# Optimization experiments

Measured on AMD Instinct MI355X. Metric: run time of the kernel, lower is better.

## Reference

```python
import jax, jax.numpy as jnp
import numpy as np

D_MODEL = 1024
NUM_HEADS = 16
ROPE_THETA = 10000.0


def setup_inputs() -> dict:
    key = jax.random.key(0)
    ks = jax.random.split(key, 5)
    B, S, D = 4, 2048, D_MODEL
    std = (2.0 / (D * D)) ** 0.5
    return {
        "x": jax.random.normal(ks[0], (B, S, D), dtype=jnp.float32),
        "Wq": jax.random.normal(ks[1], (D, D), dtype=jnp.float32) * std,
        "Wk": jax.random.normal(ks[2], (D, D), dtype=jnp.float32) * std,
        "Wv": jax.random.normal(ks[3], (D, D), dtype=jnp.float32) * std,
        "Wo": jax.random.normal(ks[4], (D, D), dtype=jnp.float32) * std,
    }


def _apply_rope(t, sin, cos):
    # t: [B, H, S, d_k]; sin/cos: [S, d_k//2] (broadcast over B, H)
    e = t[..., 0::2]
    o = t[..., 1::2]
    rot = jnp.stack((e * cos - o * sin, e * sin + o * cos), axis=-1)
    return rot.reshape(t.shape)  # interleave back to d_k


def reference(x, Wq, Wk, Wv, Wo):
    B, S, D = x.shape
    H = NUM_HEADS
    dk = D // H

    def proj(W):
        y = jnp.einsum('bsd,ed->bse', x, W)  # Linear: weight is [out, in]
        return y.reshape(B, S, H, dk).transpose(0, 2, 1, 3)  # [B,H,S,dk]

    q, k, v = proj(Wq), proj(Wk), proj(Wv)

    # RoPE cache (token_positions = arange(S))
    half = dk // 2
    inv_freq = 1.0 / (ROPE_THETA ** (jnp.arange(half, dtype=jnp.float32) * 2.0 / dk))
    angles = jnp.arange(S, dtype=jnp.float32)[:, None] * inv_freq[None, :]  # [S, half]
    sin, cos = jnp.sin(angles), jnp.cos(angles)
    q = _apply_rope(q, sin, cos)
    k = _apply_rope(k, sin, cos)

    # scaled dot-product attention with causal mask
    scores = jnp.einsum('bhqd,bhkd->bhqk', q, k) / jnp.sqrt(jnp.float32(dk))
    causal = jnp.tril(jnp.ones((S, S), dtype=bool))
    scores = jnp.where(causal, scores, jnp.finfo(scores.dtype).min)
    p = jax.nn.softmax(scores, axis=-1)
    out = jnp.einsum('bhqk,bhkd->bhqd', p, v)  # [B,H,S,dk]

    out = out.transpose(0, 2, 1, 3).reshape(B, S, D)
    return jnp.einsum('bsd,ed->bse', out, Wo)
```

## Files before the change

### kernel.cpp

```cpp
#include <hip/hip_runtime.h>

typedef unsigned short u16;
typedef unsigned int   u32;

typedef short    short8 __attribute__((ext_vector_type(8)));
typedef __bf16   bf16x8 __attribute__((ext_vector_type(8)));
typedef _Float16 half8  __attribute__((ext_vector_type(8)));
typedef float    f32x4  __attribute__((ext_vector_type(4)));

#define S_LEN   2048
#define DM      1024
#define NHEAD   16
#define DK      64
#define KDIM    1024

__device__ __forceinline__ u16 f2bf(float f) {
    u32 u = __builtin_bit_cast(u32, f);
    u += 0x7FFFu + ((u >> 16) & 1u);
    return (u16)(u >> 16);
}
__device__ __forceinline__ f32x4 mfma_bf16(short8 a, short8 b, f32x4 c) {
    return __builtin_amdgcn_mfma_f32_16x16x32_bf16(
        __builtin_bit_cast(bf16x8, a), __builtin_bit_cast(bf16x8, b), c, 0, 0, 0);
}
__device__ __forceinline__ f32x4 mfma_f16(half8 a, half8 b, f32x4 c) {
    return __builtin_amdgcn_mfma_f32_16x16x32_f16(a, b, c, 0, 0, 0);
}
__device__ __forceinline__ u32 pk_f16(float a, float b) {
    return __builtin_bit_cast(u32, __builtin_amdgcn_cvt_pkrtz(a, b));
}
__device__ __forceinline__ void gl_lds16(const void* g, void* l) {
    __builtin_amdgcn_global_load_lds(
        (const __attribute__((address_space(1))) u32*)g,
        (__attribute__((address_space(3))) u32*)l, 16, 0, 0);
}
__device__ __forceinline__ void bar_raw() { asm volatile("s_barrier" ::: "memory"); }
__device__ __forceinline__ void wait_vm2() { asm volatile("s_waitcnt vmcnt(2)" ::: "memory"); }
__device__ __forceinline__ void wait_vm0() { asm volatile("s_waitcnt vmcnt(0)" ::: "memory"); }

__device__ __forceinline__ int perm_inv(int rc) {
    const int nt = rc >> 4, mid = (rc >> 2) & 3, r = rc & 3;
    return 32 * (nt >> 1) + 8 * mid + 4 * (nt & 1) + r;
}

__global__ void cvt_all(const float4* __restrict__ x,  const float4* __restrict__ Wq,
                        const float4* __restrict__ Wk, const float4* __restrict__ Wv,
                        const float4* __restrict__ Wo,
                        uint2* __restrict__ oX, uint2* __restrict__ oWcat,
                        uint2* __restrict__ oWo,
                        float* __restrict__ sT, float* __restrict__ cT) {
    const int i = blockIdx.x * 256 + threadIdx.x;
    if (i < 3145728) {
        const float4* in;
        uint2* out;
        if (i < 2097152) {
            in = x + i;  out = oX + i;
        } else {
            const int j = i - 2097152;
            const int w = j >> 18, k = j & 262143;
            in  = (w == 0 ? Wq : w == 1 ? Wk : w == 2 ? Wv : Wo) + k;
            out = (w < 3) ? (oWcat + w * 262144 + k) : (oWo + k);
        }
        float4 f = *in;
        uint2 o;
        o.x = (u32)f2bf(f.x) | ((u32)f2bf(f.y) << 16);
        o.y = (u32)f2bf(f.z) | ((u32)f2bf(f.w) << 16);
        *out = o;
    } else {
        const int idx = i - 3145728;
        const float fi = expf(-(float)(idx >> 11) * 0.287823136624255f);
        const float ang = (float)(idx & 2047) * fi;
        sT[idx] = sinf(ang);
        cT[idx] = cosf(ang);
    }
}

template <int MODE>
__global__ __launch_bounds__(256)
void gemm_nt(const u16* __restrict__ A, const u16* __restrict__ Bw,
             u16* __restrict__ oQ, u16* __restrict__ oK, u16* __restrict__ oVt,
             float* __restrict__ oF,
             const float* __restrict__ ropeS, const float* __restrict__ ropeC) {
    __shared__ u16 As[2][128 * 32];
    __shared__ u16 Bs[2][128 * 32];
    const int tid  = threadIdx.x;
    const int wave = tid >> 6, lane = tid & 63;
    const int quad = lane >> 4, l15 = lane & 15;
    const int wr = wave >> 1, wc = wave & 1;
    const int NX  = (MODE == 0) ? 24 : 8;
    const int lin = (int)blockIdx.x + NX * (int)blockIdx.y;
    const int xcd = lin & 7, idx = lin >> 3;
    const int mbase = (xcd * 8 + idx / NX) * 128;
    const int nbase = (idx % NX) * 128;

    f32x4 acc[4][4];
#pragma unroll
    for (int i = 0; i < 4; i++)
#pragma unroll
        for (int j = 0; j < 4; j++) acc[i][j] = (f32x4)0.0f;

    const int srow0 = wave * 32 + (lane >> 2);
    const int srow1 = srow0 + 16;
    const int scolb = ((lane & 3) ^ ((lane >> 3) & 3)) * 16;
    const int ldsOff = wave * 2048 + lane * 16;
    const u16* gA0 = A  + (size_t)(mbase + srow0) * KDIM;
    const u16* gA1 = A  + (size_t)(mbase + srow1) * KDIM;
    const u16* gB0 = Bw + (size_t)(nbase + srow0) * KDIM;
    const u16* gB1 = Bw + (size_t)(nbase + srow1) * KDIM;
    const int koffq = (quad ^ ((l15 >> 1) & 3)) * 8;

    const int KT = KDIM / 64;
    for (int kt = 0; kt < KT; kt++) {
        const int kk = kt * 64;
        __syncthreads();
#pragma unroll
        for (int s = 0; s < 2; s++) {
            const int ko = kk + s * 32;
            gl_lds16((const char*)(gA0 + ko) + scolb, (char*)As[s] + ldsOff);
            gl_lds16((const char*)(gA1 + ko) + scolb, (char*)As[s] + ldsOff + 1024);
            gl_lds16((const char*)(gB0 + ko) + scolb, (char*)Bs[s] + ldsOff);
            gl_lds16((const char*)(gB1 + ko) + scolb, (char*)Bs[s] + ldsOff + 1024);
        }
        __syncthreads();

        short8 af[4][2], bf[4][2];
#pragma unroll
        for (int s = 0; s < 2; s++) {
#pragma unroll
            for (int mt = 0; mt < 4; mt++)
                af[mt][s] = *(const short8*)&As[s][(wr * 64 + mt * 16 + l15) * 32 + koffq];
#pragma unroll
            for (int nt = 0; nt < 4; nt++)
                bf[nt][s] = *(const short8*)&Bs[s][(wc * 64 + nt * 16 + l15) * 32 + koffq];
        }
#pragma unroll
        for (int s = 0; s < 2; s++)
#pragma unroll
            for (int mt = 0; mt < 4; mt++)
#pragma unroll
                for (int nt = 0; nt < 4; nt++)
                    acc[mt][nt] = mfma_bf16(af[mt][s], bf[nt][s], acc[mt][nt]);
    }

    const int proj_blk = (MODE == 0) ? (nbase >> 10) : 2;

    const float* sB[4];
    const float* cB[4];
    if (MODE == 0 && proj_blk < 2) {
#pragma unroll
        for (int nt = 0; nt < 4; nt++) {
            const int fi = nt * 8 + (l15 >> 1);
            sB[nt] = ropeS + fi * 2048;
            cB[nt] = ropeC + fi * 2048;
        }
    }
    const int par = l15 & 1;

#pragma unroll
    for (int mt = 0; mt < 4; mt++) {
#pragma unroll
        for (int nt = 0; nt < 4; nt++) {
            const int n  = nbase + wc * 64 + nt * 16 + l15;
            const int mb = mbase + wr * 64 + mt * 16 + quad * 4;
            f32x4 v = acc[mt][nt];
            if (MODE == 0) {
                const int e = n & 1023;
                const int h = e >> 6, d = e & 63;
                if (proj_blk == 2) {
                    const int b_ = mb >> 11, s = mb & 2047;
                    const int bh = b_ * NHEAD + h;
                    uint2 pk;
                    pk.x = pk_f16(v[0], v[1]);
                    pk.y = pk_f16(v[2], v[3]);
                    *(uint2*)&oVt[((size_t)bh * DK + d) * S_LEN + s] = pk;
                } else {
                    u16* dst = (proj_blk == 0) ? oQ : oK;
                    float vp[4];
#pragma unroll
                    for (int r = 0; r < 4; r++) vp[r] = __shfl_xor(v[r], 1);
                    const int b_ = mb >> 11, s0 = mb & 2047;
                    const int bh = b_ * NHEAD + h;
                    const f32x4 sn = *(const f32x4*)(sB[nt] + s0);
                    const f32x4 cs = *(const f32x4*)(cB[nt] + s0);
#pragma unroll
                    for (int r = 0; r < 4; r++) {
                        const float res = par ? (vp[r] * sn[r] + v[r] * cs[r])
                                              : (v[r] * cs[r] - vp[r] * sn[r]);
                        dst[((size_t)bh * S_LEN + (s0 + r)) * DK + d] = f2bf(res);
                    }
                }
            } else {
#pragma unroll
                for (int r = 0; r < 4; r++)
                    oF[(size_t)(mb + r) * DM + n] = v[r];
            }
        }
    }
}

__global__ __launch_bounds__(512)
void flash_attn(const u16* __restrict__ Q, const u16* __restrict__ K,
                const u16* __restrict__ Vt, u16* __restrict__ Oc) {
    __shared__ u16 Ks[2][64 * 64];
    __shared__ u16 Vs[2][64 * 64];
    const int lin = (int)blockIdx.x + 64 * (int)blockIdx.y;
    const int xcd = lin & 7, idx = lin >> 3;
    const int bh  = xcd * 8 + (idx & 7);
    const int qt  = 15 - (idx >> 3);
    const int tid  = threadIdx.x;
    const int wave = tid >> 6, lane = tid & 63;
    const int hh   = wave >> 2, w4 = wave & 3;
    const int quad = lane >> 4, l15 = lane & 15;
    const int x7 = l15 & 7;
    const size_t headQK = (size_t)bh * S_LEN * DK;
    const size_t headVt = (size_t)bh * DK * S_LEN;
    const int b = bh >> 4, h = bh & 15;
    const float SCL = 0.18033688011112042f;
    const float THRESH = 44.3614195558365f;

    half8 ones;
#pragma unroll
    for (int j = 0; j < 8; j++) ones[j] = (_Float16)1.0f;

    const int rwl  = lane >> 3;
    const int scol = (lane & 7) ^ rwl;
    const int rc   = wave * 8 + rwl;
    const u16* gK = K  + headQK + (size_t)perm_inv(rc) * DK + scol * 8;
    const u16* gV = Vt + headVt + (size_t)rc * S_LEN + scol * 8;
    const int ldsOff = wave * 1024 + lane * 16;
    const int koff0 = (quad ^ x7) * 8;
    const int koff1 = ((4 + quad) ^ x7) * 8;

    short8 qf0, qf1;
    {
        const int qrow = qt * 128 + hh * 64 + w4 * 16 + l15;
        qf0 = *(const short8*)&Q[headQK + (size_t)qrow * DK + quad * 8];
        qf1 = *(const short8*)&Q[headQK + (size_t)qrow * DK + 32 + quad * 8];
    }

    float m_st = -__builtin_inff();
    f32x4 lacc = (f32x4)0.0f;
    f32x4 oacc[4];
#pragma unroll
    for (int n = 0; n < 4; n++) oacc[n] = (f32x4)0.0f;

    const int NT = 2 * qt + 2;
    const int skip_kt = (hh == 0) ? (2 * qt + 1) : -1;
    const int diag_kt = 2 * qt + hh;
    gl_lds16(gK, (char*)Ks[0] + ldsOff);
    gl_lds16(gV, (char*)Vs[0] + ldsOff);

    for (int kt = 0; kt < NT; kt++) {
        const int cur = kt & 1, nxt = cur ^ 1;
        bar_raw();
        {
            const int ktn = (kt + 1 < NT) ? kt + 1 : kt;
            gl_lds16(gK + (size_t)ktn * 64 * DK, (char*)Ks[nxt] + ldsOff);
            gl_lds16(gV + ktn * 64,              (char*)Vs[nxt] + ldsOff);
        }
        wait_vm2();
        bar_raw();

        if (kt == skip_kt) continue;

        f32x4 sc[4];
        __builtin_amdgcn_s_setprio(1);
#pragma unroll
        for (int nt = 0; nt < 4; nt++) {
            const int rb = (nt * 16 + l15) * 64;
            short8 kf0 = *(const short8*)&Ks[cur][rb + koff0];
            short8 kf1 = *(const short8*)&Ks[cur][rb + koff1];
            f32x4 z = (f32x4)0.0f;
            z = mfma_bf16(kf0, qf0, z);
            z = mfma_bf16(kf1, qf1, z);
            sc[nt] = z;
        }
        __builtin_amdgcn_s_setprio(0);

        if (kt == diag_kt) {
            const int qloc = w4 * 16 + l15;
#pragma unroll
            for (int nt = 0; nt < 4; nt++) {
                const int kb = 32 * (nt >> 1) + 8 * quad + 4 * (nt & 1);
#pragma unroll
                for (int r = 0; r < 4; r++)
                    if (kb + r > qloc) sc[nt][r] = -__builtin_inff();
            }
        }
        float mx0 = fmaxf(fmaxf(sc[0][0], sc[0][1]), fmaxf(sc[0][2], sc[0][3]));
        float mx1 = fmaxf(fmaxf(sc[1][0], sc[1][1]), fmaxf(sc[1][2], sc[1][3]));
        float mx2 = fmaxf(fmaxf(sc[2][0], sc[2][1]), fmaxf(sc[2][2], sc[2][3]));
        float mx3 = fmaxf(fmaxf(sc[3][0], sc[3][1]), fmaxf(sc[3][2], sc[3][3]));
        float mx = fmaxf(fmaxf(mx0, mx1), fmaxf(mx2, mx3));
        mx = fmaxf(mx, __shfl_xor(mx, 16));
        mx = fmaxf(mx, __shfl_xor(mx, 32));
        if (!__all(mx - m_st <= THRESH)) {
            const float mn = fmaxf(m_st, mx);
            const float alpha = __builtin_amdgcn_exp2f((m_st - mn) * SCL);
            m_st = mn;
            float alr[4];
#pragma unroll
            for (int r = 0; r < 4; r++) alr[r] = __shfl(alpha, quad * 20 + r);
#pragma unroll
            for (int n = 0; n < 4; n++)
#pragma unroll
                for (int r = 0; r < 4; r++) oacc[n][r] *= alr[r];
#pragma unroll
            for (int r = 0; r < 4; r++) lacc[r] *= alr[r];
        }
        const float msc = m_st * SCL;
#pragma unroll
        for (int nt = 0; nt < 4; nt++)
#pragma unroll
            for (int r = 0; r < 4; r++)
                sc[nt][r] = __builtin_amdgcn_exp2f(
                    __builtin_fmaf(sc[nt][r], SCL, -msc));
        u32 pw[8];
        pw[0] = pk_f16(sc[0][0], sc[0][1]); pw[1] = pk_f16(sc[0][2], sc[0][3]);
        pw[2] = pk_f16(sc[1][0], sc[1][1]); pw[3] = pk_f16(sc[1][2], sc[1][3]);
        pw[4] = pk_f16(sc[2][0], sc[2][1]); pw[5] = pk_f16(sc[2][2], sc[2][3]);
        pw[6] = pk_f16(sc[3][0], sc[3][1]); pw[7] = pk_f16(sc[3][2], sc[3][3]);
        half8 pf0 = __builtin_bit_cast(half8, *(uint4*)&pw[0]);
        half8 pf1 = __builtin_bit_cast(half8, *(uint4*)&pw[4]);

        __builtin_amdgcn_s_setprio(1);
#pragma unroll
        for (int c = 0; c < 2; c++) {
            const half8 pf = c ? pf1 : pf0;
            lacc = mfma_f16(pf, ones, lacc);
            const int voff = ((c * 4 + quad) ^ x7) * 8;
#pragma unroll
            for (int nt2 = 0; nt2 < 4; nt2++) {
                half8 vf = __builtin_bit_cast(half8,
                    *(const short8*)&Vs[cur][(nt2 * 16 + l15) * 64 + voff]);
                oacc[nt2] = mfma_f16(pf, vf, oacc[nt2]);
            }
        }
        __builtin_amdgcn_s_setprio(0);
    }
    wait_vm0();

#pragma unroll
    for (int r = 0; r < 4; r++) {
        const float inv = 1.0f / lacc[r];
        const int s = qt * 128 + hh * 64 + w4 * 16 + quad * 4 + r;
#pragma unroll
        for (int nt2 = 0; nt2 < 4; nt2++)
            Oc[((size_t)(b * S_LEN + s)) * DM + h * 64 + nt2 * 16 + l15] =
                f2bf(oacc[nt2][r] * inv);
    }
}

#define OFF_XBF   ((size_t)0)
#define OFF_WCAT  ((size_t)8388608)
#define OFF_WO    ((size_t)11534336)
#define OFF_QB    ((size_t)12582912)
#define OFF_KB    ((size_t)20971520)
#define OFF_VT    ((size_t)29360128)
#define OFF_ROPE  ((size_t)37748736)

extern "C" void kernel_launch(void* const* d_in, const int* in_sizes, int n_in,
                              void* d_out, int out_size, void* d_ws, size_t ws_size,
                              hipStream_t stream) {
    const float* x  = (const float*)d_in[0];
    const float* Wq = (const float*)d_in[1];
    const float* Wk = (const float*)d_in[2];
    const float* Wv = (const float*)d_in[3];
    const float* Wo = (const float*)d_in[4];
    u16* ws  = (u16*)d_ws;
    u16* XBF = ws + OFF_XBF;
    u16* WCA = ws + OFF_WCAT;
    u16* WOB = ws + OFF_WO;
    u16* QB  = ws + OFF_QB;
    u16* KB  = ws + OFF_KB;
    u16* VT  = ws + OFF_VT;
    float* ropeS = (float*)(ws + OFF_ROPE);
    float* ropeC = ropeS + 65536;
    u16* AT  = XBF;

    cvt_all<<<12544, 256, 0, stream>>>((const float4*)x, (const float4*)Wq,
                                       (const float4*)Wk, (const float4*)Wv,
                                       (const float4*)Wo,
                                       (uint2*)XBF, (uint2*)WCA, (uint2*)WOB,
                                       ropeS, ropeC);

    gemm_nt<0><<<dim3(24, 64), 256, 0, stream>>>(XBF, WCA, QB, KB, VT, nullptr,
                                                 ropeS, ropeC);
    flash_attn<<<dim3(64, 16), 512, 0, stream>>>(QB, KB, VT, AT);
    gemm_nt<1><<<dim3(8, 64), 256, 0, stream>>>(AT, WOB, nullptr, nullptr, nullptr,
                                                (float*)d_out, nullptr, nullptr);
}
```

Measured before the change: 245.8 us.

## Triple-buffer K/V tiles in flash attention with one barrier per iteration

```diff
diff --git a/kernel.cpp b/kernel.cpp
--- a/kernel.cpp
+++ b/kernel.cpp
@@ -201,8 +201,8 @@
 __global__ __launch_bounds__(512)
 void flash_attn(const u16* __restrict__ Q, const u16* __restrict__ K,
                 const u16* __restrict__ Vt, u16* __restrict__ Oc) {
-    __shared__ u16 Ks[2][64 * 64];
-    __shared__ u16 Vs[2][64 * 64];
+    __shared__ u16 Ks[3][64 * 64];
+    __shared__ u16 Vs[3][64 * 64];
     const int lin = (int)blockIdx.x + 64 * (int)blockIdx.y;
     const int xcd = lin & 7, idx = lin >> 3;
     const int bh  = xcd * 8 + (idx & 7);
@@ -249,96 +249,98 @@
     const int diag_kt = 2 * qt + hh;
     gl_lds16(gK, (char*)Ks[0] + ldsOff);
     gl_lds16(gV, (char*)Vs[0] + ldsOff);
-
+    gl_lds16(gK + (size_t)64 * DK, (char*)Ks[1] + ldsOff);
+    gl_lds16(gV + 64,              (char*)Vs[1] + ldsOff);
+
+    int cur = 0, stg = 2;
     for (int kt = 0; kt < NT; kt++) {
-        const int cur = kt & 1, nxt = cur ^ 1;
+        if (kt + 1 < NT) wait_vm2(); else wait_vm0();
         bar_raw();
-        {
-            const int ktn = (kt + 1 < NT) ? kt + 1 : kt;
-            gl_lds16(gK + (size_t)ktn * 64 * DK, (char*)Ks[nxt] + ldsOff);
-            gl_lds16(gV + ktn * 64,              (char*)Vs[nxt] + ldsOff);
-        }
-        wait_vm2();
-        bar_raw();
-
-        if (kt == skip_kt) continue;
-
-        f32x4 sc[4];
-        __builtin_amdgcn_s_setprio(1);
-#pragma unroll
-        for (int nt = 0; nt < 4; nt++) {
-            const int rb = (nt * 16 + l15) * 64;
-            short8 kf0 = *(const short8*)&Ks[cur][rb + koff0];
-            short8 kf1 = *(const short8*)&Ks[cur][rb + koff1];
-            f32x4 z = (f32x4)0.0f;
-            z = mfma_bf16(kf0, qf0, z);
-            z = mfma_bf16(kf1, qf1, z);
-            sc[nt] = z;
-        }
-        __builtin_amdgcn_s_setprio(0);
-
-        if (kt == diag_kt) {
-            const int qloc = w4 * 16 + l15;
+        if (kt + 2 < NT) {
+            gl_lds16(gK + (size_t)(kt + 2) * 64 * DK, (char*)Ks[stg] + ldsOff);
+            gl_lds16(gV + (size_t)(kt + 2) * 64,      (char*)Vs[stg] + ldsOff);
+        }
+
+        if (kt != skip_kt) {
+            f32x4 sc[4];
+            __builtin_amdgcn_s_setprio(1);
 #pragma unroll
             for (int nt = 0; nt < 4; nt++) {
-                const int kb = 32 * (nt >> 1) + 8 * quad + 4 * (nt & 1);
+                const int rb = (nt * 16 + l15) * 64;
+                short8 kf0 = *(const short8*)&Ks[cur][rb + koff0];
+                short8 kf1 = *(const short8*)&Ks[cur][rb + koff1];
+                f32x4 z = (f32x4)0.0f;
+                z = mfma_bf16(kf0, qf0, z);
+                z = mfma_bf16(kf1, qf1, z);
+                sc[nt] = z;
+            }
+            __builtin_amdgcn_s_setprio(0);
+
+            if (kt == diag_kt) {
+                const int qloc = w4 * 16 + l15;
+#pragma unroll
+                for (int nt = 0; nt < 4; nt++) {
+                    const int kb = 32 * (nt >> 1) + 8 * quad + 4 * (nt & 1);
+#pragma unroll
+                    for (int r = 0; r < 4; r++)
+                        if (kb + r > qloc) sc[nt][r] = -__builtin_inff();
+                }
+            }
+            float mx0 = fmaxf(fmaxf(fmaxf(sc[0][0], sc[0][1]), sc[0][2]), sc[0][3]);
+            float mx1 = fmaxf(fmaxf(fmaxf(sc[1][0], sc[1][1]), sc[1][2]), sc[1][3]);
+            float mx2 = fmaxf(fmaxf(fmaxf(sc[2][0], sc[2][1]), sc[2][2]), sc[2][3]);
+            float mx3 = fmaxf(fmaxf(fmaxf(sc[3][0], sc[3][1]), sc[3][2]), sc[3][3]);
+            float mx = fmaxf(fmaxf(fmaxf(mx0, mx1), mx2), mx3);
+            mx = fmaxf(mx, __shfl_xor(mx, 16));
+            mx = fmaxf(mx, __shfl_xor(mx, 32));
+            if (!__all(mx - m_st <= THRESH)) {
+                const float mn = fmaxf(m_st, mx);
+                const float alpha = __builtin_amdgcn_exp2f((m_st - mn) * SCL);
+                m_st = mn;
+                float alr[4];
+#pragma unroll
+                for (int r = 0; r < 4; r++) alr[r] = __shfl(alpha, quad * 20 + r);
+#pragma unroll
+                for (int n = 0; n < 4; n++)
+#pragma unroll
+                    for (int r = 0; r < 4; r++) oacc[n][r] *= alr[r];
+#pragma unroll
+                for (int r = 0; r < 4; r++) lacc[r] *= alr[r];
+            }
+            const float msc = m_st * SCL;
+#pragma unroll
+            for (int nt = 0; nt < 4; nt++)
 #pragma unroll
                 for (int r = 0; r < 4; r++)
-                    if (kb + r > qloc) sc[nt][r] = -__builtin_inff();
-            }
-        }
-        float mx0 = fmaxf(fmaxf(sc[0][0], sc[0][1]), fmaxf(sc[0][2], sc[0][3]));
-        float mx1 = fmaxf(fmaxf(sc[1][0], sc[1][1]), fmaxf(sc[1][2], sc[1][3]));
-        float mx2 = fmaxf(fmaxf(sc[2][0], sc[2][1]), fmaxf(sc[2][2], sc[2][3]));
-        float mx3 = fmaxf(fmaxf(sc[3][0], sc[3][1]), fmaxf(sc[3][2], sc[3][3]));
-        float mx = fmaxf(fmaxf(mx0, mx1), fmaxf(mx2, mx3));
-        mx = fmaxf(mx, __shfl_xor(mx, 16));
-        mx = fmaxf(mx, __shfl_xor(mx, 32));
-        if (!__all(mx - m_st <= THRESH)) {
-            const float mn = fmaxf(m_st, mx);
-            const float alpha = __builtin_amdgcn_exp2f((m_st - mn) * SCL);
-            m_st = mn;
-            float alr[4];
-#pragma unroll
-            for (int r = 0; r < 4; r++) alr[r] = __shfl(alpha, quad * 20 + r);
-#pragma unroll
-            for (int n = 0; n < 4; n++)
-#pragma unroll
-                for (int r = 0; r < 4; r++) oacc[n][r] *= alr[r];
-#pragma unroll
-            for (int r = 0; r < 4; r++) lacc[r] *= alr[r];
-        }
-        const float msc = m_st * SCL;
-#pragma unroll
-        for (int nt = 0; nt < 4; nt++)
-#pragma unroll
-            for (int r = 0; r < 4; r++)
-                sc[nt][r] = __builtin_amdgcn_exp2f(
-                    __builtin_fmaf(sc[nt][r], SCL, -msc));
-        u32 pw[8];
-        pw[0] = pk_f16(sc[0][0], sc[0][1]); pw[1] = pk_f16(sc[0][2], sc[0][3]);
-        pw[2] = pk_f16(sc[1][0], sc[1][1]); pw[3] = pk_f16(sc[1][2], sc[1][3]);
-        pw[4] = pk_f16(sc[2][0], sc[2][1]); pw[5] = pk_f16(sc[2][2], sc[2][3]);
-        pw[6] = pk_f16(sc[3][0], sc[3][1]); pw[7] = pk_f16(sc[3][2], sc[3][3]);
-        half8 pf0 = __builtin_bit_cast(half8, *(uint4*)&pw[0]);
-        half8 pf1 = __builtin_bit_cast(half8, *(uint4*)&pw[4]);
-
-        __builtin_amdgcn_s_setprio(1);
-#pragma unroll
-        for (int c = 0; c < 2; c++) {
-            const half8 pf = c ? pf1 : pf0;
-            lacc = mfma_f16(pf, ones, lacc);
-            const int voff = ((c * 4 + quad) ^ x7) * 8;
-#pragma unroll
-            for (int nt2 = 0; nt2 < 4; nt2++) {
-                half8 vf = __builtin_bit_cast(half8,
-                    *(const short8*)&Vs[cur][(nt2 * 16 + l15) * 64 + voff]);
-                oacc[nt2] = mfma_f16(pf, vf, oacc[nt2]);
-            }
-        }
-        __builtin_amdgcn_s_setprio(0);
-    }
-    wait_vm0();
+                    sc[nt][r] = __builtin_amdgcn_exp2f(
+                        __builtin_fmaf(sc[nt][r], SCL, -msc));
+            u32 pw[8];
+            pw[0] = pk_f16(sc[0][0], sc[0][1]); pw[1] = pk_f16(sc[0][2], sc[0][3]);
+            pw[2] = pk_f16(sc[1][0], sc[1][1]); pw[3] = pk_f16(sc[1][2], sc[1][3]);
+            pw[4] = pk_f16(sc[2][0], sc[2][1]); pw[5] = pk_f16(sc[2][2], sc[2][3]);
+            pw[6] = pk_f16(sc[3][0], sc[3][1]); pw[7] = pk_f16(sc[3][2], sc[3][3]);
+            half8 pf0 = __builtin_bit_cast(half8, *(uint4*)&pw[0]);
+            half8 pf1 = __builtin_bit_cast(half8, *(uint4*)&pw[4]);
+
+            __builtin_amdgcn_s_setprio(1);
+#pragma unroll
+            for (int c = 0; c < 2; c++) {
+                const half8 pf = c ? pf1 : pf0;
+                lacc = mfma_f16(pf, ones, lacc);
+                const int voff = ((c * 4 + quad) ^ x7) * 8;
+#pragma unroll
+                for (int nt2 = 0; nt2 < 4; nt2++) {
+                    half8 vf = __builtin_bit_cast(half8,
+                        *(const short8*)&Vs[cur][(nt2 * 16 + l15) * 64 + voff]);
+                    oacc[nt2] = mfma_f16(pf, vf, oacc[nt2]);
+                }
+            }
+            __builtin_amdgcn_s_setprio(0);
+        }
+
+        cur = (cur == 2) ? 0 : cur + 1;
+        stg = (stg == 2) ? 0 : stg + 1;
+    }
 
 #pragma unroll
     for (int r = 0; r < 4; r++) {
```

After: 246.6 us. About the same (+0.3%).
